# Performance work log

Hardware: AMD Instinct MI355X
Metric: run time of the kernel (lower is better)

## Reference

```python
import jax, jax.numpy as jnp
import numpy as np

N = 50000      # nodes
E = 800000     # edges (before self-loops)
F_IN = 128     # num_node_features
H = 128        # hidden_channels
G = 256        # graphs in batch
T = 4          # num_tasks


def setup_inputs() -> dict:
    key = jax.random.key(0)
    ks = jax.random.split(key, 12)
    x = jax.random.normal(ks[0], (N, F_IN), jnp.float32)
    edge_index = jax.random.randint(ks[1], (2, E), 0, N, dtype=jnp.int64)
    batch = jnp.sort(jax.random.randint(ks[2], (N,), 0, G, dtype=jnp.int64))
    s_in = 1.0 / np.sqrt(F_IN)
    s_h = 1.0 / np.sqrt(H)
    W1 = jax.random.normal(ks[3], (F_IN, H), jnp.float32) * s_in
    b1 = jnp.zeros((H,), jnp.float32)
    W2 = jax.random.normal(ks[4], (H, H), jnp.float32) * s_h
    b2 = jnp.zeros((H,), jnp.float32)
    Wfc = jax.random.normal(ks[5], (H, H), jnp.float32) * s_h
    bfc = jnp.zeros((H,), jnp.float32)
    Wh = jax.random.normal(ks[6], (T, H, 2), jnp.float32) * s_h
    bh = jnp.zeros((T, 2), jnp.float32)
    return {"x": x, "edge_index": edge_index, "batch": batch,
            "W1": W1, "b1": b1, "W2": W2, "b2": b2,
            "Wfc": Wfc, "bfc": bfc, "Wh": Wh, "bh": bh}


def _gcn_layer(x, W, b, src, dst, dinv):
    # GCNConv: out = D^{-1/2}(A+I)D^{-1/2} X W + b  (self-loops already in src/dst)
    h = x @ W                                    # [N, H] dense transform first (fewer edge features)
    coef = dinv[src] * dinv[dst]                 # [E+N] symmetric normalization
    msg = h[src] * coef[:, None]                 # [E+N, H] gathered messages
    out = jax.ops.segment_sum(msg, dst, num_segments=N)
    return out + b


def reference(x, edge_index, batch, W1, b1, W2, b2, Wfc, bfc, Wh, bh):
    loops = jnp.arange(N, dtype=edge_index.dtype)
    src = jnp.concatenate([edge_index[0], loops])  # [E+N]
    dst = jnp.concatenate([edge_index[1], loops])
    deg = jax.ops.segment_sum(jnp.ones_like(dst, dtype=x.dtype), dst, num_segments=N)
    dinv = jax.lax.rsqrt(deg)                      # deg >= 1 due to self-loops

    h = jax.nn.relu(_gcn_layer(x, W1, b1, src, dst, dinv))
    h = jax.nn.relu(_gcn_layer(h, W2, b2, src, dst, dinv))

    # global_mean_pool over batch ids
    sums = jax.ops.segment_sum(h, batch, num_segments=G)          # [G, H]
    cnt = jax.ops.segment_sum(jnp.ones((N,), h.dtype), batch, num_segments=G)
    pooled = sums / jnp.maximum(cnt, 1.0)[:, None]

    z = jax.nn.relu(pooled @ Wfc + bfc)                           # [G, H]
    out = jnp.einsum('gh,thc->tgc', z, Wh) + bh[:, None, :]       # [T, G, 2]
    return out
```

## Files before the change

kernel.cpp:

```cpp
#include <hip/hip_runtime.h>
#include <math.h>

constexpr int N = 50000;
constexpr int E = 800000;
constexpr int F = 128;
constexpr int G = 256;
constexpr int T = 4;

constexpr int BSH   = 5;
constexpr int BNODES= 1 << BSH;
constexpr int NBUCK = (N + BNODES - 1) / BNODES;
constexpr int CHUNK = 4096;
constexpr int NCHUNK= (E + CHUNK - 1) / CHUNK;
constexpr int SSH   = 13;

constexpr int WC_BLKS  = (F * F + 255) / 256;
constexpr int PRE_Z0   = 2 * WC_BLKS;
constexpr int PRE_ZB   = (G * F + 255) / 256;
constexpr int PRE_H0   = PRE_Z0 + PRE_ZB;
constexpr int PRE_BLKS = PRE_H0 + NCHUNK;

constexpr int GB1 = (N + 63) / 64;
constexpr int GFB = GB1 + NCHUNK;
constexpr int AGB = N / 16;

typedef __attribute__((ext_vector_type(8))) short short8;
typedef __attribute__((ext_vector_type(4))) float floatx4;

__device__ inline float bf2f(unsigned short u) {
    union { unsigned int i; float f; } v;
    v.i = ((unsigned int)u) << 16;
    return v.f;
}
__device__ inline unsigned short f2bf(float f) {
    union { float f; unsigned int i; } v;
    v.f = f;
    unsigned int r = v.i + 0x7FFF + ((v.i >> 16) & 1);
    return (unsigned short)(r >> 16);
}
__device__ inline unsigned int pack2bf(float a, float b) {
    return (unsigned int)f2bf(a) | ((unsigned int)f2bf(b) << 16);
}

__device__ inline void wcast_one(const float* __restrict__ W,
                                 unsigned short* __restrict__ Whi,
                                 unsigned short* __restrict__ Wlo, int i) {
    if (i >= F * F) return;
    int k = i >> 7, n = i & 127;
    float w = W[i];
    unsigned short hi = f2bf(w);
    unsigned short lo = f2bf(w - bf2f(hi));
    int s = k >> 5, q = (k >> 3) & 3, j = k & 7;
    int idx = (((s * 128 + n) * 4 + q) * 8) + j;
    Whi[idx] = hi;
    Wlo[idx] = lo;
}

__global__ __launch_bounds__(256) void k_pre(const float* __restrict__ W1, const float* __restrict__ W2,
                                             unsigned short* __restrict__ w1h, unsigned short* __restrict__ w1l,
                                             unsigned short* __restrict__ w2h, unsigned short* __restrict__ w2l,
                                             const int* __restrict__ dst, int* __restrict__ cnts,
                                             float* __restrict__ pooled) {
    __shared__ int h[NBUCK];
    int b = blockIdx.x, t = threadIdx.x;
    if (b < WC_BLKS) {
        wcast_one(W1, w1h, w1l, b * 256 + t);
    } else if (b < 2 * WC_BLKS) {
        wcast_one(W2, w2h, w2l, (b - WC_BLKS) * 256 + t);
    } else if (b < PRE_H0) {
        pooled[(b - PRE_Z0) * 256 + t] = 0.f;
    } else {
        int chunk = b - PRE_H0;
        for (int i = t; i < NBUCK; i += 256) h[i] = 0;
        __syncthreads();
        int base = chunk * CHUNK;
        for (int i = t; i < CHUNK; i += 256) {
            int e = base + i;
            if (e < E) atomicAdd(&h[dst[e] >> BSH], 1);
        }
        __syncthreads();
        for (int i = t; i < NBUCK; i += 256) cnts[chunk * NBUCK + i] = h[i];
    }
}

__global__ __launch_bounds__(256) void k_colscan(int* __restrict__ cnts, int* __restrict__ btot) {
    __shared__ int part[256];
    int j = blockIdx.x, t = threadIdx.x;
    int k0 = 2 * t, k1 = 2 * t + 1;
    int v0 = (k0 < NCHUNK) ? cnts[k0 * NBUCK + j] : 0;
    int v1 = (k1 < NCHUNK) ? cnts[k1 * NBUCK + j] : 0;
    int s = v0 + v1;
    part[t] = s;
    __syncthreads();
    for (int off = 1; off < 256; off <<= 1) {
        int u = (t >= off) ? part[t - off] : 0;
        __syncthreads();
        part[t] += u;
        __syncthreads();
    }
    int excl = part[t] - s;
    if (k0 < NCHUNK) cnts[k0 * NBUCK + j] = excl;
    if (k1 < NCHUNK) cnts[k1 * NBUCK + j] = excl + v0;
    if (t == 255) btot[j] = part[255];
}

__global__ __launch_bounds__(256) void k_gemmfill(const float* __restrict__ x,
                                                  const unsigned short* __restrict__ w1h,
                                                  const unsigned short* __restrict__ w1l,
                                                  unsigned short* __restrict__ tmp16,
                                                  const int* __restrict__ src,
                                                  const int* __restrict__ dst,
                                                  const int* __restrict__ cnts,
                                                  const int* __restrict__ btot,
                                                  int* __restrict__ bucketbase,
                                                  unsigned int* __restrict__ staging) {
    __shared__ __align__(16) int smem[NBUCK + 1 + 256 + NBUCK];
    int b = blockIdx.x, t = threadIdx.x;
    if (b < GB1) {
        int wv = t >> 6;
        int lane = t & 63;
        int c16 = lane & 15;
        int q = lane >> 4;
        int arow = b * 64 + wv * 16 + c16;

        short8 afr[4];
        if (arow < N) {
            const float4* xr = (const float4*)(x + (size_t)arow * 128);
#pragma unroll
            for (int s = 0; s < 4; ++s) {
                float4 v0 = xr[s * 8 + q * 2];
                float4 v1 = xr[s * 8 + q * 2 + 1];
                short8 a;
                a[0] = (short)f2bf(v0.x); a[1] = (short)f2bf(v0.y);
                a[2] = (short)f2bf(v0.z); a[3] = (short)f2bf(v0.w);
                a[4] = (short)f2bf(v1.x); a[5] = (short)f2bf(v1.y);
                a[6] = (short)f2bf(v1.z); a[7] = (short)f2bf(v1.w);
                afr[s] = a;
            }
        } else {
#pragma unroll
            for (int s = 0; s < 4; ++s) afr[s] = (short8){0,0,0,0,0,0,0,0};
        }

        floatx4 acc[8];
#pragma unroll
        for (int nt = 0; nt < 8; ++nt) acc[nt] = (floatx4){0.f, 0.f, 0.f, 0.f};

        const short8* WH = (const short8*)w1h;
        const short8* WL = (const short8*)w1l;
#pragma unroll
        for (int s = 0; s < 4; ++s) {
            int wb = s * 512 + c16 * 4 + q;
#pragma unroll
            for (int nt = 0; nt < 8; ++nt) {
                acc[nt] = __builtin_amdgcn_mfma_f32_16x16x32_bf16(afr[s], WH[wb + nt * 64], acc[nt], 0, 0, 0);
                acc[nt] = __builtin_amdgcn_mfma_f32_16x16x32_bf16(afr[s], WL[wb + nt * 64], acc[nt], 0, 0, 0);
            }
        }

        int rbase = b * 64 + wv * 16 + q * 4;
#pragma unroll
        for (int r = 0; r < 4; ++r) {
            int row = rbase + r;
            if (row < N) {
#pragma unroll
                for (int nt = 0; nt < 8; ++nt)
                    tmp16[row * 128 + nt * 16 + c16] = f2bf(acc[nt][r]);
            }
        }
        return;
    }
    int* bb   = smem;
    int* part = bb + (NBUCK + 1);
    int* lofs = part + 256;
    int chunk = b - GB1;

    constexpr int CH = (NBUCK + 255) / 256;
    int beg = t * CH;
    int end = (beg + CH < NBUCK) ? beg + CH : NBUCK;
    int tot[CH];
    int s = 0;
    for (int i = beg; i < end; ++i) {
        tot[i - beg] = btot[i];
        s += btot[i];
    }
    part[t] = s;
    __syncthreads();
    for (int off = 1; off < 256; off <<= 1) {
        int u = (t >= off) ? part[t - off] : 0;
        __syncthreads();
        part[t] += u;
        __syncthreads();
    }
    int run = (t == 0) ? 0 : part[t - 1];
    for (int i = beg; i < end; ++i) {
        bb[i] = run;
        run += tot[i - beg];
    }
    if (t == 255) bb[NBUCK] = part[255];
    __syncthreads();
    if (chunk == 0)
        for (int i = t; i <= NBUCK; i += 256) bucketbase[i] = bb[i];

    for (int i = t; i < NBUCK; i += 256)
        lofs[i] = bb[i] + cnts[chunk * NBUCK + i];
    __syncthreads();

    int base = chunk * CHUNK;
    for (int i = t; i < CHUNK; i += 256) {
        int e = base + i;
        if (e < E) {
            int d = dst[e];
            int pos = atomicAdd(&lofs[d >> BSH], 1);
            staging[pos] = (unsigned int)src[e] | ((unsigned int)(d & (BNODES - 1)) << 16);
        }
    }
}

__global__ __launch_bounds__(256) void k_passB(const unsigned int* __restrict__ staging,
                                               const int* __restrict__ bucketbase,
                                               int* __restrict__ csr,
                                               int* __restrict__ rowstart,
                                               float* __restrict__ dinv,
                                               unsigned short* __restrict__ tmp16) {
    __shared__ unsigned int ent[1024];
    __shared__ int h[BNODES * 8], off_a[BNODES * 8];
    __shared__ int nodebase[BNODES], ndeg[BNODES];
    __shared__ float sdinv[BNODES];
    int b = blockIdx.x, t = threadIdx.x;
    int jb = bucketbase[b], je = bucketbase[b + 1];
    int M = je - jb;
    if (M > 1024) M = 1024;
    if (t < BNODES * 8) h[t] = 0;
    __syncthreads();

    for (int i = t; i < M; i += 256) {
        unsigned int en = staging[jb + i];
        ent[i] = en;
        int key = (((en >> 16) & (BNODES - 1)) << 3) | ((en & 0xFFFFu) >> SSH);
        atomicAdd(&h[key], 1);
    }
    __syncthreads();

    if (t < BNODES) {
        int s = 0;
#pragma unroll
        for (int c = 0; c < 8; ++c) s += h[t * 8 + c];
        ndeg[t] = s;
    }
    __syncthreads();
    if (t == 0) {
        int run = jb;
        for (int k = 0; k < BNODES; ++k) {
            nodebase[k] = run;
            run += ndeg[k];
        }
    }
    __syncthreads();
    if (t < BNODES) {
        int run = nodebase[t];
#pragma unroll
        for (int c = 0; c < 8; ++c) {
            off_a[t * 8 + c] = run;
            run += h[t * 8 + c];
        }
        float dv = rsqrtf((float)(ndeg[t] + 1));
        sdinv[t] = dv;
        int node = b * BNODES + t;
        if (node < N) {
            rowstart[node] = nodebase[t];
            dinv[node] = dv;
        }
    }
    if (b == 0 && t == 0) rowstart[N] = E;
    __syncthreads();

    for (int i = t; i < M; i += 256) {
        unsigned int en = ent[i];
        int key = (((en >> 16) & (BNODES - 1)) << 3) | ((en & 0xFFFFu) >> SSH);
        int loc = atomicAdd(&off_a[key], 1);
        csr[loc] = (int)(en & 0xFFFFu);
    }

    uint4* t4 = (uint4*)tmp16;
    for (int i = t; i < BNODES * 16; i += 256) {
        int rl = i >> 4, qi = i & 15;
        int node = b * BNODES + rl;
        if (node < N) {
            float dv = sdinv[rl];
            uint4 u = t4[node * 16 + qi];
            uint4 o;
            o.x = pack2bf(bf2f((unsigned short)(u.x & 0xFFFFu)) * dv, bf2f((unsigned short)(u.x >> 16)) * dv);
            o.y = pack2bf(bf2f((unsigned short)(u.y & 0xFFFFu)) * dv, bf2f((unsigned short)(u.y >> 16)) * dv);
            o.z = pack2bf(bf2f((unsigned short)(u.z & 0xFFFFu)) * dv, bf2f((unsigned short)(u.z >> 16)) * dv);
            o.w = pack2bf(bf2f((unsigned short)(u.w & 0xFFFFu)) * dv, bf2f((unsigned short)(u.w >> 16)) * dv);
            t4[node * 16 + qi] = o;
        }
    }
}

__device__ inline void add8(const uint4& u, float* acc) {
    union { unsigned int i; float f; } a;
    a.i = u.x << 16;          acc[0] += a.f;
    a.i = u.x & 0xFFFF0000u;  acc[1] += a.f;
    a.i = u.y << 16;          acc[2] += a.f;
    a.i = u.y & 0xFFFF0000u;  acc[3] += a.f;
    a.i = u.z << 16;          acc[4] += a.f;
    a.i = u.z & 0xFFFF0000u;  acc[5] += a.f;
    a.i = u.w << 16;          acc[6] += a.f;
    a.i = u.w & 0xFFFF0000u;  acc[7] += a.f;
}

__device__ inline void fma8(const uint4& u, float c, float* acc) {
    union { unsigned int i; float f; } a;
    a.i = u.x << 16;          acc[0] = fmaf(a.f, c, acc[0]);
    a.i = u.x & 0xFFFF0000u;  acc[1] = fmaf(a.f, c, acc[1]);
    a.i = u.y << 16;          acc[2] = fmaf(a.f, c, acc[2]);
    a.i = u.y & 0xFFFF0000u;  acc[3] = fmaf(a.f, c, acc[3]);
    a.i = u.z << 16;          acc[4] = fmaf(a.f, c, acc[4]);
    a.i = u.z & 0xFFFF0000u;  acc[5] = fmaf(a.f, c, acc[5]);
    a.i = u.w << 16;          acc[6] = fmaf(a.f, c, acc[6]);
    a.i = u.w & 0xFFFF0000u;  acc[7] = fmaf(a.f, c, acc[7]);
}

__device__ __forceinline__ void agg_loop(const uint4* __restrict__ t8l,
                                         const int* __restrict__ csr,
                                         int jb, int je, float* acc) {
    int n8 = (je - jb) >> 3;
    int j = jb;
    if (n8 > 0) {
        int e[8];
#pragma unroll
        for (int k = 0; k < 8; ++k) e[k] = csr[j + k];
        for (int c = 0; c < n8; ++c) {
            uint4 u[8];
#pragma unroll
            for (int k = 0; k < 8; ++k) u[k] = t8l[e[k] * 16];
            j += 8;
            if (c + 1 < n8) {
#pragma unroll
                for (int k = 0; k < 8; ++k) e[k] = csr[j + k];
            }
#pragma unroll
            for (int k = 0; k < 8; ++k) add8(u[k], acc);
        }
    }
    if (j < je) {
        int e[8];
        float msk[8];
#pragma unroll
        for (int k = 0; k < 8; ++k) {
            int idx = j + k;
            e[k] = csr[idx < je ? idx : je - 1];
            msk[k] = (idx < je) ? 1.0f : 0.0f;
        }
        uint4 u[8];
#pragma unroll
        for (int k = 0; k < 8; ++k) u[k] = t8l[e[k] * 16];
#pragma unroll
        for (int k = 0; k < 8; ++k) fma8(u[k], msk[k], acc);
    }
}

__global__ __launch_bounds__(256) void k_agg1gemm(const unsigned short* __restrict__ tmp16,
                                                  const int* __restrict__ csr,
                                                  const int* __restrict__ rowstart,
                                                  const float* __restrict__ dinv,
                                                  const float* __restrict__ bias,
                                                  const unsigned short* __restrict__ w2h,
                                                  const unsigned short* __restrict__ w2l,
                                                  unsigned short* __restrict__ tmp2) {
    __shared__ __align__(16) unsigned short Albs[16 * 136];
    int tid = threadIdx.x;
    int row0 = blockIdx.x * 16;

    {
        int node = row0 + (tid >> 4);
        int lane = tid & 15;
        const uint4* t8l = (const uint4*)tmp16 + lane;
        float acc[8] = {0.f, 0.f, 0.f, 0.f, 0.f, 0.f, 0.f, 0.f};
        add8(t8l[node * 16], acc);
        agg_loop(t8l, csr, rowstart[node], rowstart[node + 1], acc);

        float di = dinv[node];
        const float4* b4 = (const float4*)bias;
        float4 ba = b4[lane * 2], bb = b4[lane * 2 + 1];
        uint4 o;
        o.x = pack2bf(fmaxf(fmaf(acc[0], di, ba.x), 0.f), fmaxf(fmaf(acc[1], di, ba.y), 0.f));
        o.y = pack2bf(fmaxf(fmaf(acc[2], di, ba.z), 0.f), fmaxf(fmaf(acc[3], di, ba.w), 0.f));
        o.z = pack2bf(fmaxf(fmaf(acc[4], di, bb.x), 0.f), fmaxf(fmaf(acc[5], di, bb.y), 0.f));
        o.w = pack2bf(fmaxf(fmaf(acc[6], di, bb.z), 0.f), fmaxf(fmaf(acc[7], di, bb.w), 0.f));
        *(uint4*)&Albs[(tid >> 4) * 136 + lane * 8] = o;
    }
    __syncthreads();

    int wv = tid >> 6;
    int lane = tid & 63;
    int c16 = lane & 15;
    int q = lane >> 4;

    floatx4 acc[2];
    acc[0] = (floatx4){0.f, 0.f, 0.f, 0.f};
    acc[1] = (floatx4){0.f, 0.f, 0.f, 0.f};

    const short8* WH = (const short8*)w2h;
    const short8* WL = (const short8*)w2l;
#pragma unroll
    for (int s = 0; s < 4; ++s) {
        short8 a = *(const short8*)&Albs[c16 * 136 + s * 32 + q * 8];
        int wb = s * 512 + c16 * 4 + q;
#pragma unroll
        for (int i = 0; i < 2; ++i) {
            int nt = wv * 2 + i;
            acc[i] = __builtin_amdgcn_mfma_f32_16x16x32_bf16(a, WH[wb + nt * 64], acc[i], 0, 0, 0);
            acc[i] = __builtin_amdgcn_mfma_f32_16x16x32_bf16(a, WL[wb + nt * 64], acc[i], 0, 0, 0);
        }
    }

    int rbase = row0 + q * 4;
#pragma unroll
    for (int r = 0; r < 4; ++r) {
        int row = rbase + r;
        float dv = dinv[row];
#pragma unroll
        for (int i = 0; i < 2; ++i) {
            int nt = wv * 2 + i;
            tmp2[row * 128 + nt * 16 + c16] = f2bf(acc[i][r] * dv);
        }
    }
}

__global__ __launch_bounds__(256) void k_agg(const unsigned short* __restrict__ tmp16,
                                             const int* __restrict__ csr,
                                             const int* __restrict__ rowstart,
                                             const float* __restrict__ dinv,
                                             const float* __restrict__ bias,
                                             const int* __restrict__ batch,
                                             float* __restrict__ pooled) {
    __shared__ float red[16][128];
    __shared__ int gid[16];
    int tid = threadIdx.x;
    int node0 = blockIdx.x * 16;
    int ns = tid >> 4, lane = tid & 15;
    int node = node0 + ns;
    const uint4* t8l = (const uint4*)tmp16 + lane;
    float acc[8] = {0.f, 0.f, 0.f, 0.f, 0.f, 0.f, 0.f, 0.f};
    add8(t8l[node * 16], acc);
    agg_loop(t8l, csr, rowstart[node], rowstart[node + 1], acc);

    float di = dinv[node];
    const float4* b4 = (const float4*)bias;
    float4 ba = b4[lane * 2], bb = b4[lane * 2 + 1];
    red[ns][lane * 8 + 0] = fmaxf(fmaf(acc[0], di, ba.x), 0.f);
    red[ns][lane * 8 + 1] = fmaxf(fmaf(acc[1], di, ba.y), 0.f);
    red[ns][lane * 8 + 2] = fmaxf(fmaf(acc[2], di, ba.z), 0.f);
    red[ns][lane * 8 + 3] = fmaxf(fmaf(acc[3], di, ba.w), 0.f);
    red[ns][lane * 8 + 4] = fmaxf(fmaf(acc[4], di, bb.x), 0.f);
    red[ns][lane * 8 + 5] = fmaxf(fmaf(acc[5], di, bb.y), 0.f);
    red[ns][lane * 8 + 6] = fmaxf(fmaf(acc[6], di, bb.z), 0.f);
    red[ns][lane * 8 + 7] = fmaxf(fmaf(acc[7], di, bb.w), 0.f);
    if (tid < 16) gid[tid] = batch[node0 + tid];
    __syncthreads();

    if (tid < 128) {
        int f = tid;
        float run = 0.f;
        int g = gid[0];
        for (int r = 0; r < 16; ++r) {
            if (gid[r] != g) {
                atomicAdd(&pooled[g * 128 + f], run);
                run = 0.f;
                g = gid[r];
            }
            run += red[r][f];
        }
        atomicAdd(&pooled[g * 128 + f], run);
    }
}

__global__ __launch_bounds__(128) void k_poolhead(const float* __restrict__ pooled,
                                                  const int* __restrict__ batch,
                                                  const float* __restrict__ Wfc,
                                                  const float* __restrict__ bfc,
                                                  const float* __restrict__ Wh,
                                                  const float* __restrict__ bh,
                                                  float* __restrict__ out) {
    __shared__ float p[128];
    __shared__ float zs[128];
    int g = blockIdx.x, t = threadIdx.x;

    int lo = 0, hi = N;
    while (lo < hi) { int m = (lo + hi) >> 1; if (batch[m] < g) lo = m + 1; else hi = m; }
    int lo1 = lo, hi1 = N;
    while (lo1 < hi1) { int m = (lo1 + hi1) >> 1; if (batch[m] < g + 1) lo1 = m + 1; else hi1 = m; }
    int cnt = lo1 - lo;
    float inv = 1.0f / (float)((cnt > 1) ? cnt : 1);

    p[t] = pooled[g * 128 + t] * inv;
    __syncthreads();

    float a = bfc[t];
    for (int k = 0; k < F; ++k) a = fmaf(p[k], Wfc[k * F + t], a);
    zs[t] = fmaxf(a, 0.f);
    __syncthreads();

    if (t < T * 2) {
        int task = t >> 1, c = t & 1;
        float a2 = bh[task * 2 + c];
        const float* wr = &Wh[task * F * 2 + c];
        for (int h = 0; h < F; ++h) a2 = fmaf(zs[h], wr[h * 2], a2);
        out[task * (G * 2) + g * 2 + c] = a2;
    }
}

extern "C" void kernel_launch(void* const* d_in, const int* in_sizes, int n_in,
                              void* d_out, int out_size, void* d_ws, size_t ws_size,
                              hipStream_t stream) {
    const float* x    = (const float*)d_in[0];
    const int*   ei   = (const int*)d_in[1];
    const int*   batch= (const int*)d_in[2];
    const float* W1   = (const float*)d_in[3];
    const float* b1   = (const float*)d_in[4];
    const float* W2   = (const float*)d_in[5];
    const float* b2   = (const float*)d_in[6];
    const float* Wfc  = (const float*)d_in[7];
    const float* bfc  = (const float*)d_in[8];
    const float* Wh   = (const float*)d_in[9];
    const float* bh   = (const float*)d_in[10];
    float* out = (float*)d_out;

    const int* srcp = ei;
    const int* dstp = ei + E;

    char* w = (char*)d_ws;
    auto alloc = [&](size_t bytes) {
        char* p = w;
        w += (bytes + 255) & ~(size_t)255;
        return p;
    };
    unsigned short* tmp16 = (unsigned short*)alloc((size_t)N * F * 2);
    unsigned short* tmp2  = (unsigned short*)alloc((size_t)N * F * 2);
    int*   csr      = (int*)  alloc((size_t)E * 4);
    unsigned int* staging = (unsigned int*)alloc((size_t)E * 4);
    int*   cnts     = (int*)  alloc((size_t)NCHUNK * NBUCK * 4);
    int*   btot     = (int*)  alloc((size_t)NBUCK * 4);
    int*   bucketbase=(int*)  alloc((size_t)(NBUCK + 1) * 4);
    int*   rowstart = (int*)  alloc((size_t)(N + 1) * 4);
    float* dinv     = (float*)alloc((size_t)N * 4);
    float* pooled   = (float*)alloc((size_t)G * F * 4);
    unsigned short* w1h = (unsigned short*)alloc((size_t)F * F * 2);
    unsigned short* w1l = (unsigned short*)alloc((size_t)F * F * 2);
    unsigned short* w2h = (unsigned short*)alloc((size_t)F * F * 2);
    unsigned short* w2l = (unsigned short*)alloc((size_t)F * F * 2);

    k_pre<<<PRE_BLKS, 256, 0, stream>>>(W1, W2, w1h, w1l, w2h, w2l, dstp, cnts, pooled);

    k_colscan<<<NBUCK, 256, 0, stream>>>(cnts, btot);

    k_gemmfill<<<GFB, 256, 0, stream>>>(x, w1h, w1l, tmp16, srcp, dstp, cnts, btot,
                                        bucketbase, staging);

    k_passB<<<NBUCK, 256, 0, stream>>>(staging, bucketbase, csr, rowstart, dinv, tmp16);

    k_agg1gemm<<<AGB, 256, 0, stream>>>(tmp16, csr, rowstart, dinv, b1, w2h, w2l, tmp2);

    k_agg<<<AGB, 256, 0, stream>>>(tmp2, csr, rowstart, dinv, b2, batch, pooled);

    k_poolhead<<<G, 128, 0, stream>>>(pooled, batch, Wfc, bfc, Wh, bh, out);
}
```

Baseline: 207.0 us.

## Merge preprocessing kernels into one cooperative persistent kernel with grid syncs

Replaces the four preprocessing launches (weight cast and histogram, column scan, GEMM plus bucket fill, CSR pass B) with a single cooperative kernel of 512 blocks. The blocks loop over the old work items and separate the phases with grid.sync. This removes three kernel launch gaps and inter-kernel drains. In exchange it adds grid-wide barrier cost, and each phase is limited to a fixed grid that may leave some CUs busier than others. If the cooperative launch fails, the code falls back to the original four launches.

```diff
diff --git a/kernel.cpp b/kernel.cpp
--- a/kernel.cpp
+++ b/kernel.cpp
@@ -1,5 +1,8 @@
 #include <hip/hip_runtime.h>
+#include <hip/hip_cooperative_groups.h>
 #include <math.h>
+
+namespace cg = cooperative_groups;
 
 constexpr int N = 50000;
 constexpr int E = 800000;
@@ -14,15 +17,17 @@
 constexpr int NCHUNK= (E + CHUNK - 1) / CHUNK;
 constexpr int SSH   = 13;
 
-constexpr int WC_BLKS  = (F * F + 255) / 256;
-constexpr int PRE_Z0   = 2 * WC_BLKS;
-constexpr int PRE_ZB   = (G * F + 255) / 256;
-constexpr int PRE_H0   = PRE_Z0 + PRE_ZB;
-constexpr int PRE_BLKS = PRE_H0 + NCHUNK;
-
 constexpr int GB1 = (N + 63) / 64;
 constexpr int GFB = GB1 + NCHUNK;
 constexpr int AGB = N / 16;
+
+constexpr int MP_W2  = 64;
+constexpr int MP_Z0  = 128;
+constexpr int MP_H0  = 256;
+constexpr int MP_END = MP_H0 + NCHUNK;
+constexpr int MGRID  = 512;
+
+constexpr int PRE_BLKS = MP_END;
 
 typedef __attribute__((ext_vector_type(8))) short short8;
 typedef __attribute__((ext_vector_type(4))) float floatx4;
@@ -56,6 +61,280 @@
     Wlo[idx] = lo;
 }
 
+__device__ __forceinline__ void gemm_tile(const float* __restrict__ x,
+                                          const unsigned short* __restrict__ w1h,
+                                          const unsigned short* __restrict__ w1l,
+                                          unsigned short* __restrict__ tmp16,
+                                          int tile, int t) {
+    int wv = t >> 6;
+    int lane = t & 63;
+    int c16 = lane & 15;
+    int q = lane >> 4;
+    int arow = tile * 64 + wv * 16 + c16;
+
+    short8 afr[4];
+    if (arow < N) {
+        const float4* xr = (const float4*)(x + (size_t)arow * 128);
+#pragma unroll
+        for (int s = 0; s < 4; ++s) {
+            float4 v0 = xr[s * 8 + q * 2];
+            float4 v1 = xr[s * 8 + q * 2 + 1];
+            short8 a;
+            a[0] = (short)f2bf(v0.x); a[1] = (short)f2bf(v0.y);
+            a[2] = (short)f2bf(v0.z); a[3] = (short)f2bf(v0.w);
+            a[4] = (short)f2bf(v1.x); a[5] = (short)f2bf(v1.y);
+            a[6] = (short)f2bf(v1.z); a[7] = (short)f2bf(v1.w);
+            afr[s] = a;
+        }
+    } else {
+#pragma unroll
+        for (int s = 0; s < 4; ++s) afr[s] = (short8){0,0,0,0,0,0,0,0};
+    }
+
+    floatx4 acc[8];
+#pragma unroll
+    for (int nt = 0; nt < 8; ++nt) acc[nt] = (floatx4){0.f, 0.f, 0.f, 0.f};
+
+    const short8* WH = (const short8*)w1h;
+    const short8* WL = (const short8*)w1l;
+#pragma unroll
+    for (int s = 0; s < 4; ++s) {
+        int wb = s * 512 + c16 * 4 + q;
+#pragma unroll
+        for (int nt = 0; nt < 8; ++nt) {
+            acc[nt] = __builtin_amdgcn_mfma_f32_16x16x32_bf16(afr[s], WH[wb + nt * 64], acc[nt], 0, 0, 0);
+            acc[nt] = __builtin_amdgcn_mfma_f32_16x16x32_bf16(afr[s], WL[wb + nt * 64], acc[nt], 0, 0, 0);
+        }
+    }
+
+    int rbase = tile * 64 + wv * 16 + q * 4;
+#pragma unroll
+    for (int r = 0; r < 4; ++r) {
+        int row = rbase + r;
+        if (row < N) {
+#pragma unroll
+            for (int nt = 0; nt < 8; ++nt)
+                tmp16[row * 128 + nt * 16 + c16] = f2bf(acc[nt][r]);
+        }
+    }
+}
+
+__device__ __forceinline__ void fillb_body(char* smem, int chunk, int t,
+                                           const int* __restrict__ src,
+                                           const int* __restrict__ dst,
+                                           const int* __restrict__ cnts,
+                                           const int* __restrict__ btot,
+                                           int* __restrict__ bucketbase,
+                                           unsigned int* __restrict__ staging) {
+    int* bb   = (int*)smem;
+    int* part = (int*)(smem + 6256);
+    int* lofs = (int*)(smem + 7280);
+
+    constexpr int CH = (NBUCK + 255) / 256;
+    int beg = t * CH;
+    int end = (beg + CH < NBUCK) ? beg + CH : NBUCK;
+    int tot[CH];
+    int s = 0;
+    for (int i = beg; i < end; ++i) {
+        tot[i - beg] = btot[i];
+        s += btot[i];
+    }
+    part[t] = s;
+    __syncthreads();
+    for (int off = 1; off < 256; off <<= 1) {
+        int u = (t >= off) ? part[t - off] : 0;
+        __syncthreads();
+        part[t] += u;
+        __syncthreads();
+    }
+    int run = (t == 0) ? 0 : part[t - 1];
+    for (int i = beg; i < end; ++i) {
+        bb[i] = run;
+        run += tot[i - beg];
+    }
+    if (t == 255) bb[NBUCK] = part[255];
+    __syncthreads();
+    if (chunk == 0)
+        for (int i = t; i <= NBUCK; i += 256) bucketbase[i] = bb[i];
+
+    for (int i = t; i < NBUCK; i += 256)
+        lofs[i] = bb[i] + cnts[chunk * NBUCK + i];
+    __syncthreads();
+
+    int base = chunk * CHUNK;
+    for (int i = t; i < CHUNK; i += 256) {
+        int e = base + i;
+        if (e < E) {
+            int d = dst[e];
+            int pos = atomicAdd(&lofs[d >> BSH], 1);
+            staging[pos] = (unsigned int)src[e] | ((unsigned int)(d & (BNODES - 1)) << 16);
+        }
+    }
+}
+
+__device__ __forceinline__ void passB_body(char* smem, int bk, int t,
+                                           const unsigned int* __restrict__ staging,
+                                           const int* __restrict__ bucketbase,
+                                           int* __restrict__ csr,
+                                           int* __restrict__ rowstart,
+                                           float* __restrict__ dinv,
+                                           unsigned short* __restrict__ tmp16) {
+    unsigned int* ent = (unsigned int*)smem;
+    int* hh       = (int*)(smem + 4096);
+    int* off_a    = (int*)(smem + 5120);
+    int* nodebase = (int*)(smem + 6144);
+    int* ndeg     = (int*)(smem + 6272);
+    float* sdinv  = (float*)(smem + 6400);
+
+    int jb = bucketbase[bk], je = bucketbase[bk + 1];
+    int M = je - jb;
+    if (M > 1024) M = 1024;
+    if (t < BNODES * 8) hh[t] = 0;
+    __syncthreads();
+
+    for (int i = t; i < M; i += 256) {
+        unsigned int en = staging[jb + i];
+        ent[i] = en;
+        int key = (((en >> 16) & (BNODES - 1)) << 3) | ((en & 0xFFFFu) >> SSH);
+        atomicAdd(&hh[key], 1);
+    }
+    __syncthreads();
+
+    if (t < BNODES) {
+        int s = 0;
+#pragma unroll
+        for (int c = 0; c < 8; ++c) s += hh[t * 8 + c];
+        ndeg[t] = s;
+    }
+    __syncthreads();
+    if (t == 0) {
+        int run = jb;
+        for (int k = 0; k < BNODES; ++k) {
+            nodebase[k] = run;
+            run += ndeg[k];
+        }
+    }
+    __syncthreads();
+    if (t < BNODES) {
+        int run = nodebase[t];
+#pragma unroll
+        for (int c = 0; c < 8; ++c) {
+            off_a[t * 8 + c] = run;
+            run += hh[t * 8 + c];
+        }
+        float dv = rsqrtf((float)(ndeg[t] + 1));
+        sdinv[t] = dv;
+        int node = bk * BNODES + t;
+        if (node < N) {
+            rowstart[node] = nodebase[t];
+            dinv[node] = dv;
+        }
+    }
+    if (bk == 0 && t == 0) rowstart[N] = E;
+    __syncthreads();
+
+    for (int i = t; i < M; i += 256) {
+        unsigned int en = ent[i];
+        int key = (((en >> 16) & (BNODES - 1)) << 3) | ((en & 0xFFFFu) >> SSH);
+        int loc = atomicAdd(&off_a[key], 1);
+        csr[loc] = (int)(en & 0xFFFFu);
+    }
+
+    uint4* t4 = (uint4*)tmp16;
+    for (int i = t; i < BNODES * 16; i += 256) {
+        int rl = i >> 4, qi = i & 15;
+        int node = bk * BNODES + rl;
+        if (node < N) {
+            float dv = sdinv[rl];
+            uint4 u = t4[node * 16 + qi];
+            uint4 o;
+            o.x = pack2bf(bf2f((unsigned short)(u.x & 0xFFFFu)) * dv, bf2f((unsigned short)(u.x >> 16)) * dv);
+            o.y = pack2bf(bf2f((unsigned short)(u.y & 0xFFFFu)) * dv, bf2f((unsigned short)(u.y >> 16)) * dv);
+            o.z = pack2bf(bf2f((unsigned short)(u.z & 0xFFFFu)) * dv, bf2f((unsigned short)(u.z >> 16)) * dv);
+            o.w = pack2bf(bf2f((unsigned short)(u.w & 0xFFFFu)) * dv, bf2f((unsigned short)(u.w >> 16)) * dv);
+            t4[node * 16 + qi] = o;
+        }
+    }
+}
+
+__global__ __launch_bounds__(256) void k_merged(
+        const float* __restrict__ x, const float* __restrict__ W1, const float* __restrict__ W2,
+        unsigned short* __restrict__ w1h, unsigned short* __restrict__ w1l,
+        unsigned short* __restrict__ w2h, unsigned short* __restrict__ w2l,
+        const int* __restrict__ src, const int* __restrict__ dst,
+        int* __restrict__ cnts, int* __restrict__ btot, int* __restrict__ bucketbase,
+        unsigned int* __restrict__ staging, int* __restrict__ csr, int* __restrict__ rowstart,
+        float* __restrict__ dinv, unsigned short* __restrict__ tmp16,
+        float* __restrict__ pooled) {
+    cg::grid_group grid = cg::this_grid();
+    __shared__ __align__(16) char smem[13536];
+    int b = blockIdx.x, t = threadIdx.x;
+
+    for (int u = b; u < MP_END; u += MGRID) {
+        __syncthreads();
+        if (u < MP_W2) {
+            wcast_one(W1, w1h, w1l, u * 256 + t);
+        } else if (u < MP_Z0) {
+            wcast_one(W2, w2h, w2l, (u - MP_W2) * 256 + t);
+        } else if (u < MP_H0) {
+            pooled[(u - MP_Z0) * 256 + t] = 0.f;
+        } else {
+            int chunk = u - MP_H0;
+            int* h = (int*)smem;
+            for (int i = t; i < NBUCK; i += 256) h[i] = 0;
+            __syncthreads();
+            int base = chunk * CHUNK;
+            for (int i = t; i < CHUNK; i += 256) {
+                int e = base + i;
+                if (e < E) atomicAdd(&h[dst[e] >> BSH], 1);
+            }
+            __syncthreads();
+            for (int i = t; i < NBUCK; i += 256) cnts[chunk * NBUCK + i] = h[i];
+        }
+    }
+    __threadfence();
+    grid.sync();
+
+    for (int j = b; j < NBUCK; j += MGRID) {
+        __syncthreads();
+        int* part = (int*)smem;
+        int k0 = 2 * t, k1 = 2 * t + 1;
+        int v0 = (k0 < NCHUNK) ? cnts[k0 * NBUCK + j] : 0;
+        int v1 = (k1 < NCHUNK) ? cnts[k1 * NBUCK + j] : 0;
+        int s = v0 + v1;
+        part[t] = s;
+        __syncthreads();
+        for (int off = 1; off < 256; off <<= 1) {
+            int u = (t >= off) ? part[t - off] : 0;
+            __syncthreads();
+            part[t] += u;
+            __syncthreads();
+        }
+        int excl = part[t] - s;
+        if (k0 < NCHUNK) cnts[k0 * NBUCK + j] = excl;
+        if (k1 < NCHUNK) cnts[k1 * NBUCK + j] = excl + v0;
+        if (t == 255) btot[j] = part[255];
+    }
+    __threadfence();
+    grid.sync();
+
+    for (int u = b; u < GFB; u += MGRID) {
+        __syncthreads();
+        if (u < GB1) {
+            gemm_tile(x, w1h, w1l, tmp16, u, t);
+        } else {
+            fillb_body(smem, u - GB1, t, src, dst, cnts, btot, bucketbase, staging);
+        }
+    }
+    __threadfence();
+    grid.sync();
+
+    for (int bk = b; bk < NBUCK; bk += MGRID) {
+        __syncthreads();
+        passB_body(smem, bk, t, staging, bucketbase, csr, rowstart, dinv, tmp16);
+    }
+}
+
 __global__ __launch_bounds__(256) void k_pre(const float* __restrict__ W1, const float* __restrict__ W2,
                                              unsigned short* __restrict__ w1h, unsigned short* __restrict__ w1l,
                                              unsigned short* __restrict__ w2h, unsigned short* __restrict__ w2l,
@@ -63,14 +342,14 @@
                                              float* __restrict__ pooled) {
     __shared__ int h[NBUCK];
     int b = blockIdx.x, t = threadIdx.x;
-    if (b < WC_BLKS) {
+    if (b < MP_W2) {
         wcast_one(W1, w1h, w1l, b * 256 + t);
-    } else if (b < 2 * WC_BLKS) {
-        wcast_one(W2, w2h, w2l, (b - WC_BLKS) * 256 + t);
-    } else if (b < PRE_H0) {
-        pooled[(b - PRE_Z0) * 256 + t] = 0.f;
+    } else if (b < MP_Z0) {
+        wcast_one(W2, w2h, w2l, (b - MP_W2) * 256 + t);
+    } else if (b < MP_H0) {
+        pooled[(b - MP_Z0) * 256 + t] = 0.f;
     } else {
-        int chunk = b - PRE_H0;
+        int chunk = b - MP_H0;
         for (int i = t; i < NBUCK; i += 256) h[i] = 0;
         __syncthreads();
         int base = chunk * CHUNK;
@@ -114,107 +393,13 @@
                                                   const int* __restrict__ btot,
                                                   int* __restrict__ bucketbase,
                                                   unsigned int* __restrict__ staging) {
-    __shared__ __align__(16) int smem[NBUCK + 1 + 256 + NBUCK];
+    __shared__ __align__(16) char smem[13536];
     int b = blockIdx.x, t = threadIdx.x;
     if (b < GB1) {
-        int wv = t >> 6;
-        int lane = t & 63;
-        int c16 = lane & 15;
-        int q = lane >> 4;
-        int arow = b * 64 + wv * 16 + c16;
-
-        short8 afr[4];
-        if (arow < N) {
-            const float4* xr = (const float4*)(x + (size_t)arow * 128);
-#pragma unroll
-            for (int s = 0; s < 4; ++s) {
-                float4 v0 = xr[s * 8 + q * 2];
-                float4 v1 = xr[s * 8 + q * 2 + 1];
-                short8 a;
-                a[0] = (short)f2bf(v0.x); a[1] = (short)f2bf(v0.y);
-                a[2] = (short)f2bf(v0.z); a[3] = (short)f2bf(v0.w);
-                a[4] = (short)f2bf(v1.x); a[5] = (short)f2bf(v1.y);
-                a[6] = (short)f2bf(v1.z); a[7] = (short)f2bf(v1.w);
-                afr[s] = a;
-            }
-        } else {
-#pragma unroll
-            for (int s = 0; s < 4; ++s) afr[s] = (short8){0,0,0,0,0,0,0,0};
-        }
-
-        floatx4 acc[8];
-#pragma unroll
-        for (int nt = 0; nt < 8; ++nt) acc[nt] = (floatx4){0.f, 0.f, 0.f, 0.f};
-
-        const short8* WH = (const short8*)w1h;
-        const short8* WL = (const short8*)w1l;
-#pragma unroll
-        for (int s = 0; s < 4; ++s) {
-            int wb = s * 512 + c16 * 4 + q;
-#pragma unroll
-            for (int nt = 0; nt < 8; ++nt) {
-                acc[nt] = __builtin_amdgcn_mfma_f32_16x16x32_bf16(afr[s], WH[wb + nt * 64], acc[nt], 0, 0, 0);
-                acc[nt] = __builtin_amdgcn_mfma_f32_16x16x32_bf16(afr[s], WL[wb + nt * 64], acc[nt], 0, 0, 0);
-            }
-        }
-
-        int rbase = b * 64 + wv * 16 + q * 4;
-#pragma unroll
-        for (int r = 0; r < 4; ++r) {
-            int row = rbase + r;
-            if (row < N) {
-#pragma unroll
-                for (int nt = 0; nt < 8; ++nt)
-                    tmp16[row * 128 + nt * 16 + c16] = f2bf(acc[nt][r]);
-            }
-        }
+        gemm_tile(x, w1h, w1l, tmp16, b, t);
         return;
     }
-    int* bb   = smem;
-    int* part = bb + (NBUCK + 1);
-    int* lofs = part + 256;
-    int chunk = b - GB1;
-
-    constexpr int CH = (NBUCK + 255) / 256;
-    int beg = t * CH;
-    int end = (beg + CH < NBUCK) ? beg + CH : NBUCK;
-    int tot[CH];
-    int s = 0;
-    for (int i = beg; i < end; ++i) {
-        tot[i - beg] = btot[i];
-        s += btot[i];
-    }
-    part[t] = s;
-    __syncthreads();
-    for (int off = 1; off < 256; off <<= 1) {
-        int u = (t >= off) ? part[t - off] : 0;
-        __syncthreads();
-        part[t] += u;
-        __syncthreads();
-    }
-    int run = (t == 0) ? 0 : part[t - 1];
-    for (int i = beg; i < end; ++i) {
-        bb[i] = run;
-        run += tot[i - beg];
-    }
-    if (t == 255) bb[NBUCK] = part[255];
-    __syncthreads();
-    if (chunk == 0)
-        for (int i = t; i <= NBUCK; i += 256) bucketbase[i] = bb[i];
-
-    for (int i = t; i < NBUCK; i += 256)
-        lofs[i] = bb[i] + cnts[chunk * NBUCK + i];
-    __syncthreads();
-
-    int base = chunk * CHUNK;
-    for (int i = t; i < CHUNK; i += 256) {
-        int e = base + i;
-        if (e < E) {
-            int d = dst[e];
-            int pos = atomicAdd(&lofs[d >> BSH], 1);
-            staging[pos] = (unsigned int)src[e] | ((unsigned int)(d & (BNODES - 1)) << 16);
-        }
-    }
+    fillb_body(smem, b - GB1, t, src, dst, cnts, btot, bucketbase, staging);
 }
 
 __global__ __launch_bounds__(256) void k_passB(const unsigned int* __restrict__ staging,
@@ -223,80 +408,8 @@
                                                int* __restrict__ rowstart,
                                                float* __restrict__ dinv,
                                                unsigned short* __restrict__ tmp16) {
-    __shared__ unsigned int ent[1024];
-    __shared__ int h[BNODES * 8], off_a[BNODES * 8];
-    __shared__ int nodebase[BNODES], ndeg[BNODES];
-    __shared__ float sdinv[BNODES];
-    int b = blockIdx.x, t = threadIdx.x;
-    int jb = bucketbase[b], je = bucketbase[b + 1];
-    int M = je - jb;
-    if (M > 1024) M = 1024;
-    if (t < BNODES * 8) h[t] = 0;
-    __syncthreads();
-
-    for (int i = t; i < M; i += 256) {
-        unsigned int en = staging[jb + i];
-        ent[i] = en;
-        int key = (((en >> 16) & (BNODES - 1)) << 3) | ((en & 0xFFFFu) >> SSH);
-        atomicAdd(&h[key], 1);
-    }
-    __syncthreads();
-
-    if (t < BNODES) {
-        int s = 0;
-#pragma unroll
-        for (int c = 0; c < 8; ++c) s += h[t * 8 + c];
-        ndeg[t] = s;
-    }
-    __syncthreads();
-    if (t == 0) {
-        int run = jb;
-        for (int k = 0; k < BNODES; ++k) {
-            nodebase[k] = run;
-            run += ndeg[k];
-        }
-    }
-    __syncthreads();
-    if (t < BNODES) {
-        int run = nodebase[t];
-#pragma unroll
-        for (int c = 0; c < 8; ++c) {
-            off_a[t * 8 + c] = run;
-            run += h[t * 8 + c];
-        }
-        float dv = rsqrtf((float)(ndeg[t] + 1));
-        sdinv[t] = dv;
-        int node = b * BNODES + t;
-        if (node < N) {
-            rowstart[node] = nodebase[t];
-            dinv[node] = dv;
-        }
-    }
-    if (b == 0 && t == 0) rowstart[N] = E;
-    __syncthreads();
-
-    for (int i = t; i < M; i += 256) {
-        unsigned int en = ent[i];
-        int key = (((en >> 16) & (BNODES - 1)) << 3) | ((en & 0xFFFFu) >> SSH);
-        int loc = atomicAdd(&off_a[key], 1);
-        csr[loc] = (int)(en & 0xFFFFu);
-    }
-
-    uint4* t4 = (uint4*)tmp16;
-    for (int i = t; i < BNODES * 16; i += 256) {
-        int rl = i >> 4, qi = i & 15;
-        int node = b * BNODES + rl;
-        if (node < N) {
-            float dv = sdinv[rl];
-            uint4 u = t4[node * 16 + qi];
-            uint4 o;
-            o.x = pack2bf(bf2f((unsigned short)(u.x & 0xFFFFu)) * dv, bf2f((unsigned short)(u.x >> 16)) * dv);
-            o.y = pack2bf(bf2f((unsigned short)(u.y & 0xFFFFu)) * dv, bf2f((unsigned short)(u.y >> 16)) * dv);
-            o.z = pack2bf(bf2f((unsigned short)(u.z & 0xFFFFu)) * dv, bf2f((unsigned short)(u.z >> 16)) * dv);
-            o.w = pack2bf(bf2f((unsigned short)(u.w & 0xFFFFu)) * dv, bf2f((unsigned short)(u.w >> 16)) * dv);
-            t4[node * 16 + qi] = o;
-        }
-    }
+    __shared__ __align__(16) char smem[13536];
+    passB_body(smem, blockIdx.x, threadIdx.x, staging, bucketbase, csr, rowstart, dinv, tmp16);
 }
 
 __device__ inline void add8(const uint4& u, float* acc) {
@@ -553,14 +666,22 @@
     unsigned short* w2h = (unsigned short*)alloc((size_t)F * F * 2);
     unsigned short* w2l = (unsigned short*)alloc((size_t)F * F * 2);
 
-    k_pre<<<PRE_BLKS, 256, 0, stream>>>(W1, W2, w1h, w1l, w2h, w2l, dstp, cnts, pooled);
-
-    k_colscan<<<NBUCK, 256, 0, stream>>>(cnts, btot);
-
-    k_gemmfill<<<GFB, 256, 0, stream>>>(x, w1h, w1l, tmp16, srcp, dstp, cnts, btot,
-                                        bucketbase, staging);
-
-    k_passB<<<NBUCK, 256, 0, stream>>>(staging, bucketbase, csr, rowstart, dinv, tmp16);
+    void* kargs[] = { (void*)&x, (void*)&W1, (void*)&W2,
+                      (void*)&w1h, (void*)&w1l, (void*)&w2h, (void*)&w2l,
+                      (void*)&srcp, (void*)&dstp,
+                      (void*)&cnts, (void*)&btot, (void*)&bucketbase,
+                      (void*)&staging, (void*)&csr, (void*)&rowstart,
+                      (void*)&dinv, (void*)&tmp16, (void*)&pooled };
+    hipError_t cerr = hipLaunchCooperativeKernel((void*)k_merged, dim3(MGRID), dim3(256),
+                                                 kargs, 0, stream);
+    if (cerr != hipSuccess) {
+        (void)hipGetLastError();
+        k_pre<<<PRE_BLKS, 256, 0, stream>>>(W1, W2, w1h, w1l, w2h, w2l, dstp, cnts, pooled);
+        k_colscan<<<NBUCK, 256, 0, stream>>>(cnts, btot);
+        k_gemmfill<<<GFB, 256, 0, stream>>>(x, w1h, w1l, tmp16, srcp, dstp, cnts, btot,
+                                            bucketbase, staging);
+        k_passB<<<NBUCK, 256, 0, stream>>>(staging, bucketbase, csr, rowstart, dinv, tmp16);
+    }
 
     k_agg1gemm<<<AGB, 256, 0, stream>>>(tmp16, csr, rowstart, dinv, b1, w2h, w2l, tmp2);
 
```

Result: slower. 590.7 us (+185.3%).
